# Kernel optimization log

Measured on AMD Instinct MI355X. Metric: run time of the kernel, lower is better.

## Reference

```python
import math
import jax, jax.numpy as jnp
import numpy as np

B, N, D_FULL, M, D_V = 8, 4096, 256, 256, 256


def _phi(x, omega):
    # x: [..., N, d_full], omega: [M, d_full] -> [..., N, M]
    proj = x @ omega.T
    log_phi = proj - 0.5 * jnp.sum(x * x, axis=-1, keepdims=True)
    log_phi = log_phi - jnp.max(log_phi, axis=-1, keepdims=True)
    return jnp.exp(log_phi) / math.sqrt(omega.shape[0])


def _causal(phi_q, phi_k, V):
    # phi_q/phi_k: [B, N, M], V: [B, N, d_v]
    b, n, m = phi_q.shape
    d_v = V.shape[-1]

    def step(carry, inp):
        S, z = carry
        pq, pk, v = inp  # [B,M], [B,M], [B,d_v]
        S = S + pk[:, :, None] * v[:, None, :]          # [B, M, d_v]
        z = z + pk                                       # [B, M]
        num = jnp.einsum('bi,bij->bj', pq, S)            # [B, d_v]
        den = jnp.maximum(jnp.sum(pq * z, axis=-1), 1e-6)
        return (S, z), num / den[:, None]

    S0 = jnp.zeros((b, m, d_v), phi_q.dtype)
    z0 = jnp.zeros((b, m), phi_q.dtype)
    xs = (jnp.swapaxes(phi_q, 0, 1), jnp.swapaxes(phi_k, 0, 1), jnp.swapaxes(V, 0, 1))
    _, ys = jax.lax.scan(step, (S0, z0), xs)  # ys: [N, B, d_v]
    return jnp.swapaxes(ys, 0, 1)


def setup_inputs() -> dict:
    key = jax.random.key(0)
    kq, kk, kv, ko = jax.random.split(key, 4)
    Q = jax.random.normal(kq, (B, N, D_FULL), dtype=jnp.float32)
    K_in = jax.random.normal(kk, (B, N, D_FULL), dtype=jnp.float32)
    V = jax.random.normal(kv, (B, N, D_V), dtype=jnp.float32)
    omega = jax.random.normal(ko, (M, D_FULL), dtype=jnp.float32)
    return {"Q": Q, "K_in": K_in, "V": V, "omega": omega, "causal": 1}


def reference(Q, K_in, V, omega, causal):
    phi_q = _phi(Q, omega)
    phi_k = _phi(K_in, omega)
    if causal:
        return _causal(phi_q, phi_k, V)
    S = jnp.einsum('bni,bnj->bij', phi_k, V)          # [B, M, d_v]
    z = jnp.sum(phi_k, axis=-2)                        # [B, M]
    num = jnp.einsum('bni,bij->bnj', phi_q, S)
    den = jnp.maximum(jnp.einsum('bni,bi->bn', phi_q, z), 1e-6)
    return num / den[..., None]
```

## Files before the change

kernel.cpp:

```cpp
#include <hip/hip_runtime.h>

#define BN 8
#define NN 4096
#define DD 256
#define MM 256
#define DV 256
#define CHUNK 256
#define NC (NN / CHUNK)

using f32x4 = __attribute__((ext_vector_type(4))) float;
using s16x8 = __attribute__((ext_vector_type(8))) short;

#define MFMA16(a, b, c) __builtin_amdgcn_mfma_f32_16x16x32_bf16(a, b, c, 0, 0, 0)

__device__ __forceinline__ unsigned short f2bf(float x) {
    union { float f; unsigned int u; } v; v.f = x;
    unsigned int r = v.u + 0x7FFF + ((v.u >> 16) & 1);
    return (unsigned short)(r >> 16);
}
__device__ __forceinline__ float bf2f(unsigned short u) {
    union { unsigned int u; float f; } v; v.u = ((unsigned int)u) << 16;
    return v.f;
}

__device__ __forceinline__ void split4(const float4 x, unsigned short h[4], unsigned short l[4])
{
    const float xs[4] = {x.x, x.y, x.z, x.w};
#pragma unroll
    for (int j = 0; j < 4; ++j) {
        union { float f; unsigned u; } v; v.f = xs[j];
        const unsigned hm = v.u & 0xFFFF0000u;
        union { unsigned u; float f; } hv; hv.u = hm;
        h[j] = (unsigned short)(hm >> 16);
        l[j] = f2bf(xs[j] - hv.f);
    }
}

__global__ __launch_bounds__(256) void omconv(
    const float* __restrict__ Om, unsigned short* __restrict__ OmH,
    unsigned short* __restrict__ OmL)
{
    const int i = blockIdx.x * 256 + threadIdx.x;
    const int row = i >> 6;
    const int k0  = (i & 63) * 4;
    const float4 v = *(const float4*)(Om + (size_t)row * DD + k0);
    const int wv = row >> 6, ct = (row >> 4) & 3, colL = row & 15;
    const int kt = k0 >> 5, quad = (k0 >> 3) & 3, e0 = k0 & 7;
    const int lanep = quad * 16 + colL;
    const size_t off = ((size_t)((wv * 8 + kt) * 4 + ct) * 64 + lanep) * 8 + e0;
    unsigned short h[4], l[4];
    split4(v, h, l);
    *(uint2*)(OmH + off) = *(uint2*)h;
    *(uint2*)(OmL + off) = *(uint2*)l;
}

__global__ __launch_bounds__(256, 4) void phi_fused(
    const float* __restrict__ Qp, const float* __restrict__ Kp,
    const unsigned short* __restrict__ OmH, const unsigned short* __restrict__ OmL,
    unsigned short* __restrict__ PhiQ, unsigned short* __restrict__ PhiK,
    unsigned short* __restrict__ PhiT, float* __restrict__ Zp)
{
    const int tid = threadIdx.x;
    const int w = tid >> 6;
    const int lane = tid & 63;
    const int col = lane & 15, quad = lane >> 4;
    const bool kpath = blockIdx.x < 1024;
    const int id = kpath ? blockIdx.x : (blockIdx.x - 1024);
    const float* __restrict__ X = kpath ? Kp : Qp;
    unsigned short* __restrict__ Phi = kpath ? PhiK : PhiQ;
    const long r0 = (long)id * 32;

    __shared__ __align__(16) short AhS[32][264];
    __shared__ __align__(16) short AlS[32][264];
    __shared__ float rowmax_s[32];
    float (*red)[68] = (float(*)[68])AhS;
    unsigned short (*P)[264] = (unsigned short(*)[264])AlS;
    unsigned int* P32 = (unsigned int*)AlS;

    {
        float4 xv[8];
#pragma unroll
        for (int j = 0; j < 8; ++j) {
            const int row = w * 8 + j;
            xv[j] = *(const float4*)(X + (r0 + row) * DD + lane * 4);
        }
#pragma unroll
        for (int j = 0; j < 8; ++j) {
            const int row = w * 8 + j;
            unsigned short h[4], l[4];
            split4(xv[j], h, l);
            *(uint2*)&AhS[row][lane * 4] = *(uint2*)h;
            *(uint2*)&AlS[row][lane * 4] = *(uint2*)l;
        }
    }

    const unsigned short* OmHw = OmH + (size_t)w * 8 * 4 * 512;
    const unsigned short* OmLw = OmL + (size_t)w * 8 * 4 * 512;
    f32x4 acc[2][4] = {};
    s16x8 bh0[4], bl0[4], bh1[4], bl1[4];
#pragma unroll
    for (int ct = 0; ct < 4; ++ct) {
        const size_t off = ((size_t)ct * 64 + lane) * 8;
        bh0[ct] = *(const s16x8*)(OmHw + off);
        bl0[ct] = *(const s16x8*)(OmLw + off);
    }
    __syncthreads();

#pragma unroll
    for (int kt = 0; kt < 8; ++kt) {
        if (kt < 7) {
#pragma unroll
            for (int ct = 0; ct < 4; ++ct) {
                const size_t off = ((size_t)((kt + 1) * 4 + ct) * 64 + lane) * 8;
                bh1[ct] = *(const s16x8*)(OmHw + off);
                bl1[ct] = *(const s16x8*)(OmLw + off);
            }
        }
#pragma unroll
        for (int t = 0; t < 2; ++t) {
            const s16x8 ah = *(const s16x8*)&AhS[t * 16 + col][kt * 32 + quad * 8];
            const s16x8 al = *(const s16x8*)&AlS[t * 16 + col][kt * 32 + quad * 8];
#pragma unroll
            for (int ct = 0; ct < 4; ++ct) {
                acc[t][ct] = MFMA16(ah, bh0[ct], acc[t][ct]);
                acc[t][ct] = MFMA16(ah, bl0[ct], acc[t][ct]);
                acc[t][ct] = MFMA16(al, bh0[ct], acc[t][ct]);
            }
        }
#pragma unroll
        for (int ct = 0; ct < 4; ++ct) { bh0[ct] = bh1[ct]; bl0[ct] = bl1[ct]; }
    }

    __syncthreads();
#pragma unroll
    for (int t = 0; t < 2; ++t)
#pragma unroll
        for (int r = 0; r < 4; ++r) {
            float m = acc[t][0][r];
#pragma unroll
            for (int ct = 1; ct < 4; ++ct) m = fmaxf(m, acc[t][ct][r]);
            red[t * 16 + quad * 4 + r][w * 16 + col] = m;
        }
    __syncthreads();
    {
        const int row = tid >> 3, seg = tid & 7;
        float m = red[row][seg * 8];
#pragma unroll
        for (int j = 1; j < 8; ++j) m = fmaxf(m, red[row][seg * 8 + j]);
        m = fmaxf(m, __shfl_xor(m, 1));
        m = fmaxf(m, __shfl_xor(m, 2));
        m = fmaxf(m, __shfl_xor(m, 4));
        if (seg == 0) rowmax_s[row] = m;
    }
    __syncthreads();

#pragma unroll
    for (int t = 0; t < 2; ++t)
#pragma unroll
        for (int r = 0; r < 4; ++r) {
            const int n = t * 16 + quad * 4 + r;
            const float rm = rowmax_s[n];
#pragma unroll
            for (int ct = 0; ct < 4; ++ct) {
                const float val = __expf(acc[t][ct][r] - rm) * 0.0625f;
                const unsigned u = (unsigned)f2bf(val);
                const unsigned up = (unsigned)__shfl_xor((int)u, 1);
                if ((col & 1) == 0)
                    P32[n * 132 + w * 32 + ct * 8 + (col >> 1)] = u | (up << 16);
            }
        }
    __syncthreads();

    {
        const int t7 = tid & 7;
        const int nb = tid >> 3;
#pragma unroll
        for (int s = 0; s < 4; ++s)
            *(uint4*)(Phi + (r0 + nb) * MM + t7 * 8 + s * 64) =
                *(const uint4*)&P[nb][t7 * 8 + s * 64];
    }

    if (kpath) {
        const int b = id >> 7;
        const int c = (id >> 3) & 15;
        const int n0 = (id & 127) * 32;
        const int nb4 = (tid & 3) * 8;
        const int mBase = tid >> 2;
#pragma unroll
        for (int mi = 0; mi < 4; ++mi) {
            const int m = mi * 64 + mBase;
            unsigned short u[8];
#pragma unroll
            for (int j = 0; j < 8; ++j) u[j] = P[nb4 + j][m];
            *(uint4*)(PhiT + ((size_t)b * MM + m) * NN + n0 + nb4) = *(uint4*)u;
        }
        float z = 0.f;
#pragma unroll
        for (int n = 0; n < 32; ++n) z += bf2f(P[n][tid]);
        atomicAdd(&Zp[((b * NC + c) << 8) + tid], z);
    }
}

__global__ __launch_bounds__(256) void transpose_v(
    const float* __restrict__ V, unsigned short* __restrict__ VT)
{
    const int tid = threadIdx.x;
    const int ct = blockIdx.x & 3;
    const long r0 = (long)(blockIdx.x >> 2) * 64;
    const int b = (int)(r0 >> 12);
    const int n0 = (int)(r0 & (NN - 1));
    __shared__ unsigned short T[64][72];
    const int rr = tid >> 4, cs = tid & 15;
#pragma unroll
    for (int p = 0; p < 4; ++p) {
        const int r = p * 16 + rr;
        const float4 v = *(const float4*)(V + (r0 + r) * DV + ct * 64 + cs * 4);
        T[cs * 4 + 0][r] = f2bf(v.x); T[cs * 4 + 1][r] = f2bf(v.y);
        T[cs * 4 + 2][r] = f2bf(v.z); T[cs * 4 + 3][r] = f2bf(v.w);
    }
    __syncthreads();
    const int cl = tid >> 3, ns = tid & 7;
#pragma unroll
    for (int p = 0; p < 2; ++p) {
        const int c = p * 32 + cl;
        *(uint4*)(VT + ((size_t)b * DV + ct * 64 + c) * NN + n0 + ns * 8) = *(uint4*)&T[c][ns * 8];
    }
}

__global__ __launch_bounds__(256, 3) void state_mfma(
    const unsigned short* __restrict__ VT, const unsigned short* __restrict__ PkT,
    unsigned short* __restrict__ ST)
{
    const int tid = threadIdx.x;
    const int w = tid >> 6;
    const int lane = tid & 63;
    const int col = lane & 15, quad = lane >> 4;
    const int q  = blockIdx.x >> 7;
    const int bc = blockIdx.x & 127;
    const int c  = bc & 15;
    const int b  = bc >> 4;
    const int dv0 = (q & 1) * 128 + (w & 1) * 64;
    const int m0  = (q >> 1) * 128 + (w >> 1) * 64;
    const unsigned short* Ab = VT  + (size_t)b * DV * NN + (size_t)c * CHUNK;
    const unsigned short* Bb = PkT + (size_t)b * MM * NN + (size_t)c * CHUNK;

    f32x4 acc[4][4] = {};
    s16x8 a0[4], b0[4], a1[4], b1[4];
#pragma unroll
    for (int t = 0; t < 4; ++t) {
        a0[t] = *(const s16x8*)(Ab + (size_t)(dv0 + t * 16 + col) * NN + quad * 8);
        b0[t] = *(const s16x8*)(Bb + (size_t)(m0 + t * 16 + col) * NN + quad * 8);
    }
#pragma unroll
    for (int kt = 0; kt < 8; ++kt) {
        if (kt < 7) {
#pragma unroll
            for (int t = 0; t < 4; ++t) {
                a1[t] = *(const s16x8*)(Ab + (size_t)(dv0 + t * 16 + col) * NN + (kt + 1) * 32 + quad * 8);
                b1[t] = *(const s16x8*)(Bb + (size_t)(m0 + t * 16 + col) * NN + (kt + 1) * 32 + quad * 8);
            }
        }
#pragma unroll
        for (int i = 0; i < 4; ++i)
#pragma unroll
            for (int j = 0; j < 4; ++j) acc[i][j] = MFMA16(a0[i], b0[j], acc[i][j]);
#pragma unroll
        for (int t = 0; t < 4; ++t) { a0[t] = a1[t]; b0[t] = b1[t]; }
    }
    unsigned short* Sb = ST + (((size_t)(b * NC + c)) << 16);
#pragma unroll
    for (int i = 0; i < 4; ++i)
#pragma unroll
        for (int j = 0; j < 4; ++j)
#pragma unroll
            for (int r = 0; r < 4; ++r)
                Sb[(dv0 + i * 16 + quad * 4 + r) * MM + m0 + j * 16 + col] = f2bf(acc[i][j][r]);
}

__global__ __launch_bounds__(256) void prefix2(
    unsigned short* __restrict__ ST, float* __restrict__ Z)
{
    const long idx = (long)blockIdx.x * 256 + threadIdx.x;
    const int b = (int)(idx >> 16);
    const int r = (int)(idx & 65535);
    float run = 0.f;
#pragma unroll
    for (int c = 0; c < NC; ++c) {
        const size_t off = (((size_t)(b * NC + c)) << 16) + r;
        const float v = bf2f(ST[off]);
        ST[off] = f2bf(run);
        run += v;
    }
    if (idx < BN * MM) {
        const int b2 = (int)(idx >> 8);
        const int m = (int)(idx & 255);
        float rz = 0.f;
#pragma unroll
        for (int c = 0; c < NC; ++c) {
            const size_t off = (size_t)(b2 * NC + c) * MM + m;
            const float v = Z[off];
            Z[off] = rz;
            rz += v;
        }
    }
}

__global__ __launch_bounds__(256) void out_mfma(
    const unsigned short* __restrict__ PhiQ, const unsigned short* __restrict__ PhiK,
    const unsigned short* __restrict__ VT, const unsigned short* __restrict__ ST,
    const float* __restrict__ Z, float* __restrict__ Out)
{
    const int tid = threadIdx.x;
    const int w = tid >> 6;
    const int lane = tid & 63;
    const int col = lane & 15, quad = lane >> 4;
    const int it = 3 - (blockIdx.x >> 7);
    const int low = blockIdx.x & 127;
    const int c  = low & 15;
    const int b  = low >> 4;
    const size_t chunk_row = (size_t)b * NN + (size_t)c * CHUNK;
    const unsigned short* Qrow = PhiQ + (chunk_row + it * 64) * MM;

    __shared__ unsigned short Qs[64][264];
    __shared__ unsigned short A_s[64][72];
    __shared__ float red[64][68];
    __shared__ float z_s[256];
    __shared__ float den_s[64];

    const float zval = Z[((size_t)(b * NC + c) << 8) + tid];
    s16x8 bk0[8], bk1[8];
#pragma unroll
    for (int ms = 0; ms < 8; ++ms)
        bk0[ms] = *(const s16x8*)(PhiK + (chunk_row)*MM + (size_t)(w * 16 + col) * MM + ms * 32 + quad * 8);
    uint4 qv[8];
#pragma unroll
    for (int i = 0; i < 8; ++i)
        qv[i] = *((const uint4*)Qrow + i * 256 + tid);
    z_s[tid] = zval;
#pragma unroll
    for (int i = 0; i < 8; ++i) {
        const int f = i * 256 + tid;
        *(uint4*)&Qs[f >> 5][(f & 31) * 8] = qv[i];
    }
    __syncthreads();

    f32x4 oacc[4][4] = {};
    float rsum[4][4] = {};

    for (int jt = 0; jt <= it; ++jt) {
        s16x8 bv[8];
        const unsigned short* Vbase = VT + ((size_t)b * DV + w * 64) * NN + (size_t)c * CHUNK + jt * 64;
#pragma unroll
        for (int ks2 = 0; ks2 < 2; ++ks2)
#pragma unroll
            for (int t2 = 0; t2 < 4; ++t2)
                bv[ks2 * 4 + t2] = *(const s16x8*)(Vbase + (size_t)(t2 * 16 + col) * NN + ks2 * 32 + quad * 8);
        f32x4 accA[4] = {};
#pragma unroll
        for (int ms = 0; ms < 8; ++ms)
#pragma unroll
            for (int t = 0; t < 4; ++t) {
                const s16x8 aq = *(const s16x8*)&Qs[t * 16 + col][ms * 32 + quad * 8];
                accA[t] = MFMA16(aq, bk0[ms], accA[t]);
            }
        if (jt < it) {
            const unsigned short* Krn = PhiK + (chunk_row + (jt + 1) * 64) * MM;
#pragma unroll
            for (int ms = 0; ms < 8; ++ms)
                bk1[ms] = *(const s16x8*)(Krn + (size_t)(w * 16 + col) * MM + ms * 32 + quad * 8);
        }
        __syncthreads();
#pragma unroll
        for (int t = 0; t < 4; ++t)
#pragma unroll
            for (int r = 0; r < 4; ++r) {
                const int i_loc = t * 16 + quad * 4 + r;
                const int j_loc = w * 16 + col;
                float v = (jt * 64 + j_loc <= it * 64 + i_loc) ? accA[t][r] : 0.f;
                rsum[t][r] += v;
                A_s[i_loc][j_loc] = f2bf(v);
            }
        __syncthreads();
#pragma unroll
        for (int ks2 = 0; ks2 < 2; ++ks2) {
            s16x8 av[4];
#pragma unroll
            for (int t = 0; t < 4; ++t)
                av[t] = *(const s16x8*)&A_s[t * 16 + col][ks2 * 32 + quad * 8];
#pragma unroll
            for (int t2 = 0; t2 < 4; ++t2)
#pragma unroll
                for (int t = 0; t < 4; ++t)
                    oacc[t][t2] = MFMA16(av[t], bv[ks2 * 4 + t2], oacc[t][t2]);
        }
#pragma unroll
        for (int ms = 0; ms < 8; ++ms) bk0[ms] = bk1[ms];
    }
#pragma unroll
    for (int t = 0; t < 4; ++t)
#pragma unroll
        for (int r = 0; r < 4; ++r)
            red[t * 16 + quad * 4 + r][w * 16 + col] = rsum[t][r];

    const unsigned short* Sb = ST + (((size_t)(b * NC + c)) << 16) + (size_t)(w * 64) * MM;
    s16x8 bs0[4], bs1[4];
#pragma unroll
    for (int t2 = 0; t2 < 4; ++t2)
        bs0[t2] = *(const s16x8*)(Sb + (size_t)(t2 * 16 + col) * MM + quad * 8);
#pragma unroll
    for (int ms = 0; ms < 8; ++ms) {
        if (ms < 7) {
#pragma unroll
            for (int t2 = 0; t2 < 4; ++t2)
                bs1[t2] = *(const s16x8*)(Sb + (size_t)(t2 * 16 + col) * MM + (ms + 1) * 32 + quad * 8);
        }
        s16x8 aq[4];
#pragma unroll
        for (int t = 0; t < 4; ++t)
            aq[t] = *(const s16x8*)&Qs[t * 16 + col][ms * 32 + quad * 8];
#pragma unroll
        for (int t2 = 0; t2 < 4; ++t2)
#pragma unroll
            for (int t = 0; t < 4; ++t)
                oacc[t][t2] = MFMA16(aq[t], bs0[t2], oacc[t][t2]);
#pragma unroll
        for (int t2 = 0; t2 < 4; ++t2) bs0[t2] = bs1[t2];
    }
    {
        const int i = tid & 63;
        const int seg = tid >> 6;
        float d = 0.f;
#pragma unroll
        for (int g = 0; g < 8; ++g) {
            const s16x8 qv8 = *(const s16x8*)&Qs[i][seg * 64 + g * 8];
#pragma unroll
            for (int x = 0; x < 8; ++x)
                d = fmaf(bf2f((unsigned short)qv8[x]), z_s[seg * 64 + g * 8 + x], d);
        }
        red[i][64 + seg] = d;
    }
    __syncthreads();
    if (tid < 64) {
        float s = 0.f;
#pragma unroll
        for (int j = 0; j < 68; ++j) s += red[tid][j];
        den_s[tid] = fmaxf(s, 1e-6f);
    }
    __syncthreads();
#pragma unroll
    for (int t = 0; t < 4; ++t)
#pragma unroll
        for (int r = 0; r < 4; ++r) {
            const int i_loc = t * 16 + quad * 4 + r;
            const float invd = 1.0f / den_s[i_loc];
#pragma unroll
            for (int t2 = 0; t2 < 4; ++t2)
                Out[(chunk_row + it * 64 + i_loc) * DV + w * 64 + t2 * 16 + col] = oacc[t][t2][r] * invd;
        }
}

extern "C" void kernel_launch(void* const* d_in, const int* in_sizes, int n_in,
                              void* d_out, int out_size, void* d_ws, size_t ws_size,
                              hipStream_t stream)
{
    const float* Q  = (const float*)d_in[0];
    const float* K  = (const float*)d_in[1];
    const float* V  = (const float*)d_in[2];
    const float* Om = (const float*)d_in[3];
    float* out = (float*)d_out;

    const size_t NM = (size_t)BN * NN * MM;
    unsigned short* PhiQ  = (unsigned short*)d_ws;
    unsigned short* PhiK  = PhiQ + NM;
    unsigned short* PhiKT = PhiK + NM;
    unsigned short* VT    = PhiKT + NM;
    unsigned short* ST    = VT + NM;
    unsigned short* OmH   = ST + (size_t)BN * NC * DV * MM;
    unsigned short* OmL   = OmH + (size_t)MM * DD;
    float* Z = (float*)(OmL + (size_t)MM * DD);

    hipMemsetAsync(Z, 0, (size_t)BN * NC * MM * sizeof(float), stream);
    omconv<<<dim3(64), dim3(256), 0, stream>>>(Om, OmH, OmL);
    phi_fused<<<dim3(2048), dim3(256), 0, stream>>>(Q, K, OmH, OmL, PhiQ, PhiK, PhiKT, Z);
    transpose_v<<<dim3((BN * NN) / 64 * 4), dim3(256), 0, stream>>>(V, VT);
    state_mfma<<<dim3(BN * NC * 4), dim3(256), 0, stream>>>(VT, PhiKT, ST);
    prefix2<<<dim3((BN * DV * MM) / 256), dim3(256), 0, stream>>>(ST, Z);
    out_mfma<<<dim3(BN * NC * 4), dim3(256), 0, stream>>>(PhiQ, PhiK, VT, ST, Z, out);
}
```

Baseline: 230.7 us.

## Store PhiK, PhiK^T, V^T and S in MFMA fragment-native tiled layouts

The producer kernels (phi_fused, transpose_v, state_mfma) now write their intermediates in a per-chunk layout that matches the MFMA operand fragments. Each lane's 8-element fragment then sits at a contiguous lane-indexed offset. The consumers (state_mfma, out_mfma) load operands as fully coalesced 16-byte-per-lane reads instead of strided row reads spanning NN or MM elements. This is meant to cut uncoalesced global loads and TLB/cache pressure in the GEMM stages. The cost is more complex index math, and prefix2 must agree with the new S layout.

```diff
diff --git a/kernel.cpp b/kernel.cpp
--- a/kernel.cpp
+++ b/kernel.cpp
@@ -12,6 +12,7 @@
 using s16x8 = __attribute__((ext_vector_type(8))) short;
 
 #define MFMA16(a, b, c) __builtin_amdgcn_mfma_f32_16x16x32_bf16(a, b, c, 0, 0, 0)
+
 
 __device__ __forceinline__ unsigned short f2bf(float x) {
     union { float f; unsigned int u; } v; v.f = x;
@@ -57,8 +58,8 @@
 __global__ __launch_bounds__(256, 4) void phi_fused(
     const float* __restrict__ Qp, const float* __restrict__ Kp,
     const unsigned short* __restrict__ OmH, const unsigned short* __restrict__ OmL,
-    unsigned short* __restrict__ PhiQ, unsigned short* __restrict__ PhiK,
-    unsigned short* __restrict__ PhiT, float* __restrict__ Zp)
+    unsigned short* __restrict__ PhiQ, unsigned short* __restrict__ PhiKF,
+    unsigned short* __restrict__ PhiTF, float* __restrict__ Zp)
 {
     const int tid = threadIdx.x;
     const int w = tid >> 6;
@@ -67,7 +68,6 @@
     const bool kpath = blockIdx.x < 1024;
     const int id = kpath ? blockIdx.x : (blockIdx.x - 1024);
     const float* __restrict__ X = kpath ? Kp : Qp;
-    unsigned short* __restrict__ Phi = kpath ? PhiK : PhiQ;
     const long r0 = (long)id * 32;
 
     __shared__ __align__(16) short AhS[32][264];
@@ -171,28 +171,36 @@
         }
     __syncthreads();
 
-    {
+    if (!kpath) {
         const int t7 = tid & 7;
         const int nb = tid >> 3;
 #pragma unroll
         for (int s = 0; s < 4; ++s)
-            *(uint4*)(Phi + (r0 + nb) * MM + t7 * 8 + s * 64) =
+            *(uint4*)(PhiQ + (r0 + nb) * MM + t7 * 8 + s * 64) =
                 *(const uint4*)&P[nb][t7 * 8 + s * 64];
-    }
-
-    if (kpath) {
+    } else {
         const int b = id >> 7;
-        const int c = (id >> 3) & 15;
-        const int n0 = (id & 127) * 32;
-        const int nb4 = (tid & 3) * 8;
-        const int mBase = tid >> 2;
-#pragma unroll
-        for (int mi = 0; mi < 4; ++mi) {
-            const int m = mi * 64 + mBase;
+        const int ib = id & 127;
+        const int c = ib >> 3;
+        const size_t bc = ((size_t)(b * NC + c)) << 16;
+        const int jt = (ib >> 1) & 3;
+        const int half = ib & 1;
+        const int ktp = ib & 7;
+#pragma unroll
+        for (int p = 0; p < 4; ++p) {
+            const int msw = p * 4 + (tid >> 6);
+            const int ms = msw >> 1, wl = msw & 1;
+            const uint4 v = *(const uint4*)&P[wl * 16 + (lane & 15)][ms * 32 + (lane >> 4) * 8];
+            *(uint4*)(PhiKF + bc + (((size_t)(jt * 8 + ms) * 4 + half * 2 + wl) * 64 + lane) * 8) = v;
+        }
+#pragma unroll
+        for (int p = 0; p < 4; ++p) {
+            const int mq = p, t = tid >> 6;
             unsigned short u[8];
 #pragma unroll
-            for (int j = 0; j < 8; ++j) u[j] = P[nb4 + j][m];
-            *(uint4*)(PhiT + ((size_t)b * MM + m) * NN + n0 + nb4) = *(uint4*)u;
+            for (int e = 0; e < 8; ++e)
+                u[e] = P[(lane >> 4) * 8 + e][mq * 64 + t * 16 + (lane & 15)];
+            *(uint4*)(PhiTF + bc + (((size_t)(mq * 8 + ktp) * 4 + t) * 64 + lane) * 8) = *(uint4*)u;
         }
         float z = 0.f;
 #pragma unroll
@@ -202,13 +210,16 @@
 }
 
 __global__ __launch_bounds__(256) void transpose_v(
-    const float* __restrict__ V, unsigned short* __restrict__ VT)
+    const float* __restrict__ V, unsigned short* __restrict__ VTF)
 {
     const int tid = threadIdx.x;
     const int ct = blockIdx.x & 3;
     const long r0 = (long)(blockIdx.x >> 2) * 64;
     const int b = (int)(r0 >> 12);
     const int n0 = (int)(r0 & (NN - 1));
+    const int c = n0 >> 8;
+    const int kt0 = (n0 & 255) >> 5;
+    const size_t bc = ((size_t)(b * NC + c)) << 16;
     __shared__ unsigned short T[64][72];
     const int rr = tid >> 4, cs = tid & 15;
 #pragma unroll
@@ -219,62 +230,67 @@
         T[cs * 4 + 2][r] = f2bf(v.z); T[cs * 4 + 3][r] = f2bf(v.w);
     }
     __syncthreads();
-    const int cl = tid >> 3, ns = tid & 7;
+    const int t = (tid >> 6) & 3, lane = tid & 63;
 #pragma unroll
     for (int p = 0; p < 2; ++p) {
-        const int c = p * 32 + cl;
-        *(uint4*)(VT + ((size_t)b * DV + ct * 64 + c) * NN + n0 + ns * 8) = *(uint4*)&T[c][ns * 8];
+        const int kt2 = p;
+        const uint4 v = *(const uint4*)&T[t * 16 + (lane & 15)][kt2 * 32 + (lane >> 4) * 8];
+        *(uint4*)(VTF + bc + (((size_t)(ct * 8 + kt0 + kt2) * 4 + t) * 64 + lane) * 8) = v;
     }
 }
 
 __global__ __launch_bounds__(256, 3) void state_mfma(
-    const unsigned short* __restrict__ VT, const unsigned short* __restrict__ PkT,
-    unsigned short* __restrict__ ST)
+    const unsigned short* __restrict__ VTF, const unsigned short* __restrict__ PhiTF,
+    unsigned short* __restrict__ STF)
 {
     const int tid = threadIdx.x;
     const int w = tid >> 6;
     const int lane = tid & 63;
     const int col = lane & 15, quad = lane >> 4;
     const int q  = blockIdx.x >> 7;
-    const int bc = blockIdx.x & 127;
-    const int c  = bc & 15;
-    const int b  = bc >> 4;
-    const int dv0 = (q & 1) * 128 + (w & 1) * 64;
-    const int m0  = (q >> 1) * 128 + (w >> 1) * 64;
-    const unsigned short* Ab = VT  + (size_t)b * DV * NN + (size_t)c * CHUNK;
-    const unsigned short* Bb = PkT + (size_t)b * MM * NN + (size_t)c * CHUNK;
+    const int bci = blockIdx.x & 127;
+    const int c  = bci & 15;
+    const int b  = bci >> 4;
+    const int dvq = (q & 1) * 2 + (w & 1);
+    const int mq  = (q >> 1) * 2 + (w >> 1);
+    const size_t bc = ((size_t)(b * NC + c)) << 16;
+    const unsigned short* Af = VTF   + bc + (size_t)dvq * 16384;
+    const unsigned short* Bf = PhiTF + bc + (size_t)mq  * 16384;
 
     f32x4 acc[4][4] = {};
     s16x8 a0[4], b0[4], a1[4], b1[4];
 #pragma unroll
     for (int t = 0; t < 4; ++t) {
-        a0[t] = *(const s16x8*)(Ab + (size_t)(dv0 + t * 16 + col) * NN + quad * 8);
-        b0[t] = *(const s16x8*)(Bb + (size_t)(m0 + t * 16 + col) * NN + quad * 8);
+        a0[t] = *(const s16x8*)(Af + ((size_t)t * 64 + lane) * 8);
+        b0[t] = *(const s16x8*)(Bf + ((size_t)t * 64 + lane) * 8);
     }
 #pragma unroll
     for (int kt = 0; kt < 8; ++kt) {
         if (kt < 7) {
 #pragma unroll
             for (int t = 0; t < 4; ++t) {
-                a1[t] = *(const s16x8*)(Ab + (size_t)(dv0 + t * 16 + col) * NN + (kt + 1) * 32 + quad * 8);
-                b1[t] = *(const s16x8*)(Bb + (size_t)(m0 + t * 16 + col) * NN + (kt + 1) * 32 + quad * 8);
+                a1[t] = *(const s16x8*)(Af + ((size_t)((kt + 1) * 4 + t) * 64 + lane) * 8);
+                b1[t] = *(const s16x8*)(Bf + ((size_t)((kt + 1) * 4 + t) * 64 + lane) * 8);
             }
         }
 #pragma unroll
         for (int i = 0; i < 4; ++i)
 #pragma unroll
-            for (int j = 0; j < 4; ++j) acc[i][j] = MFMA16(a0[i], b0[j], acc[i][j]);
+            for (int j = 0; j < 4; ++j) acc[i][j] = MFMA16(b0[i], a0[j], acc[i][j]);
 #pragma unroll
         for (int t = 0; t < 4; ++t) { a0[t] = a1[t]; b0[t] = b1[t]; }
     }
-    unsigned short* Sb = ST + (((size_t)(b * NC + c)) << 16);
 #pragma unroll
     for (int i = 0; i < 4; ++i)
 #pragma unroll
-        for (int j = 0; j < 4; ++j)
-#pragma unroll
-            for (int r = 0; r < 4; ++r)
-                Sb[(dv0 + i * 16 + quad * 4 + r) * MM + m0 + j * 16 + col] = f2bf(acc[i][j][r]);
+        for (int j = 0; j < 4; ++j) {
+            unsigned short s[4];
+#pragma unroll
+            for (int r = 0; r < 4; ++r) s[r] = f2bf(acc[i][j][r]);
+            const int lanep = ((i & 1) * 2 + (quad >> 1)) * 16 + col;
+            const size_t off = (((size_t)(dvq * 8 + mq * 2 + (i >> 1)) * 4 + j) * 64 + lanep) * 8 + (quad & 1) * 4;
+            *(uint2*)(STF + bc + off) = *(uint2*)s;
+        }
 }
 
 __global__ __launch_bounds__(256) void prefix2(
@@ -306,8 +322,8 @@
 }
 
 __global__ __launch_bounds__(256) void out_mfma(
-    const unsigned short* __restrict__ PhiQ, const unsigned short* __restrict__ PhiK,
-    const unsigned short* __restrict__ VT, const unsigned short* __restrict__ ST,
+    const unsigned short* __restrict__ PhiQ, const unsigned short* __restrict__ PhiKF,
+    const unsigned short* __restrict__ VTF, const unsigned short* __restrict__ STF,
     const float* __restrict__ Z, float* __restrict__ Out)
 {
     const int tid = threadIdx.x;
@@ -319,7 +335,10 @@
     const int c  = low & 15;
     const int b  = low >> 4;
     const size_t chunk_row = (size_t)b * NN + (size_t)c * CHUNK;
+    const size_t bc = ((size_t)(b * NC + c)) << 16;
     const unsigned short* Qrow = PhiQ + (chunk_row + it * 64) * MM;
+    const unsigned short* Vf = VTF + bc + (size_t)w * 16384;
+    const unsigned short* Sf = STF + bc + (size_t)w * 16384;
 
     __shared__ unsigned short Qs[64][264];
     __shared__ unsigned short A_s[64][72];
@@ -331,7 +350,7 @@
     s16x8 bk0[8], bk1[8];
 #pragma unroll
     for (int ms = 0; ms < 8; ++ms)
-        bk0[ms] = *(const s16x8*)(PhiK + (chunk_row)*MM + (size_t)(w * 16 + col) * MM + ms * 32 + quad * 8);
+        bk0[ms] = *(const s16x8*)(PhiKF + bc + (((size_t)ms * 4 + w) * 64 + lane) * 8);
     uint4 qv[8];
 #pragma unroll
     for (int i = 0; i < 8; ++i)
@@ -349,12 +368,11 @@
 
     for (int jt = 0; jt <= it; ++jt) {
         s16x8 bv[8];
-        const unsigned short* Vbase = VT + ((size_t)b * DV + w * 64) * NN + (size_t)c * CHUNK + jt * 64;
 #pragma unroll
         for (int ks2 = 0; ks2 < 2; ++ks2)
 #pragma unroll
             for (int t2 = 0; t2 < 4; ++t2)
-                bv[ks2 * 4 + t2] = *(const s16x8*)(Vbase + (size_t)(t2 * 16 + col) * NN + ks2 * 32 + quad * 8);
+                bv[ks2 * 4 + t2] = *(const s16x8*)(Vf + (((size_t)(jt * 2 + ks2) * 4 + t2) * 64 + lane) * 8);
         f32x4 accA[4] = {};
 #pragma unroll
         for (int ms = 0; ms < 8; ++ms)
@@ -364,10 +382,9 @@
                 accA[t] = MFMA16(aq, bk0[ms], accA[t]);
             }
         if (jt < it) {
-            const unsigned short* Krn = PhiK + (chunk_row + (jt + 1) * 64) * MM;
 #pragma unroll
             for (int ms = 0; ms < 8; ++ms)
-                bk1[ms] = *(const s16x8*)(Krn + (size_t)(w * 16 + col) * MM + ms * 32 + quad * 8);
+                bk1[ms] = *(const s16x8*)(PhiKF + bc + (((size_t)((jt + 1) * 8 + ms) * 4 + w) * 64 + lane) * 8);
         }
         __syncthreads();
 #pragma unroll
@@ -402,17 +419,16 @@
         for (int r = 0; r < 4; ++r)
             red[t * 16 + quad * 4 + r][w * 16 + col] = rsum[t][r];
 
-    const unsigned short* Sb = ST + (((size_t)(b * NC + c)) << 16) + (size_t)(w * 64) * MM;
     s16x8 bs0[4], bs1[4];
 #pragma unroll
     for (int t2 = 0; t2 < 4; ++t2)
-        bs0[t2] = *(const s16x8*)(Sb + (size_t)(t2 * 16 + col) * MM + quad * 8);
+        bs0[t2] = *(const s16x8*)(Sf + ((size_t)t2 * 64 + lane) * 8);
 #pragma unroll
     for (int ms = 0; ms < 8; ++ms) {
         if (ms < 7) {
 #pragma unroll
             for (int t2 = 0; t2 < 4; ++t2)
-                bs1[t2] = *(const s16x8*)(Sb + (size_t)(t2 * 16 + col) * MM + (ms + 1) * 32 + quad * 8);
+                bs1[t2] = *(const s16x8*)(Sf + ((size_t)((ms + 1) * 4 + t2) * 64 + lane) * 8);
         }
         s16x8 aq[4];
 #pragma unroll
@@ -471,19 +487,19 @@
 
     const size_t NM = (size_t)BN * NN * MM;
     unsigned short* PhiQ  = (unsigned short*)d_ws;
-    unsigned short* PhiK  = PhiQ + NM;
-    unsigned short* PhiKT = PhiK + NM;
-    unsigned short* VT    = PhiKT + NM;
-    unsigned short* ST    = VT + NM;
-    unsigned short* OmH   = ST + (size_t)BN * NC * DV * MM;
+    unsigned short* PhiKF = PhiQ + NM;
+    unsigned short* PhiTF = PhiKF + NM;
+    unsigned short* VTF   = PhiTF + NM;
+    unsigned short* STF   = VTF + NM;
+    unsigned short* OmH   = STF + (size_t)BN * NC * DV * MM;
     unsigned short* OmL   = OmH + (size_t)MM * DD;
     float* Z = (float*)(OmL + (size_t)MM * DD);
 
     hipMemsetAsync(Z, 0, (size_t)BN * NC * MM * sizeof(float), stream);
     omconv<<<dim3(64), dim3(256), 0, stream>>>(Om, OmH, OmL);
-    phi_fused<<<dim3(2048), dim3(256), 0, stream>>>(Q, K, OmH, OmL, PhiQ, PhiK, PhiKT, Z);
-    transpose_v<<<dim3((BN * NN) / 64 * 4), dim3(256), 0, stream>>>(V, VT);
-    state_mfma<<<dim3(BN * NC * 4), dim3(256), 0, stream>>>(VT, PhiKT, ST);
-    prefix2<<<dim3((BN * DV * MM) / 256), dim3(256), 0, stream>>>(ST, Z);
-    out_mfma<<<dim3(BN * NC * 4), dim3(256), 0, stream>>>(PhiQ, PhiK, VT, ST, Z, out);
-}
+    phi_fused<<<dim3(2048), dim3(256), 0, stream>>>(Q, K, OmH, OmL, PhiQ, PhiKF, PhiTF, Z);
+    transpose_v<<<dim3((BN * NN) / 64 * 4), dim3(256), 0, stream>>>(V, VTF);
+    state_mfma<<<dim3(BN * NC * 4), dim3(256), 0, stream>>>(VTF, PhiTF, STF);
+    prefix2<<<dim3((BN * DV * MM) / 256), dim3(256), 0, stream>>>(STF, Z);
+    out_mfma<<<dim3(BN * NC * 4), dim3(256), 0, stream>>>(PhiQ, PhiKF, VTF, STF, Z, out);
+}
```

Measured after the change: 222.1 us. -3.7%, faster.
